# Performance work log

Measured on AMD Instinct MI355X. Metric: run time of the kernel, lower is better.

Reference implementation:

```python
import jax, jax.numpy as jnp
import numpy as np

B, T, D = 1, 2048, 2048
H, HKV, DH = 32, 8, 64          # head_dim = D // H, n_rep = H // HKV
NREP = H // HKV
WINDOW = 1024
NMETA = 128
EPS = 1e-6
ROPE_BASE = 10000.0


def _rmsnorm(x, w):
    # per-head-dim RMSNorm computed in float32 (matches torch module)
    xf = x.astype(jnp.float32)
    rms = jax.lax.rsqrt(jnp.mean(xf * xf, axis=-1, keepdims=True) + EPS)
    return (w * xf * rms).astype(x.dtype)


def _rope(x, pos):
    # x: [B, h, L, DH], pos: [B, L]; interleaved even/odd rotation
    inv_freq = 1.0 / (ROPE_BASE ** (jnp.arange(0, DH, 2, dtype=jnp.float32) / DH))
    freqs = pos.astype(jnp.float32)[..., None] * inv_freq        # [B, L, DH/2]
    cos = jnp.cos(freqs)[:, None]                                # [B, 1, L, DH/2]
    sin = jnp.sin(freqs)[:, None]
    x1, x2 = x[..., ::2], x[..., 1::2]
    rot = jnp.stack([x1 * cos - x2 * sin, x1 * sin + x2 * cos], axis=-1)
    return rot.reshape(x.shape)


def setup_inputs() -> dict:
    key = jax.random.key(0)
    ks = jax.random.split(key, 5)
    s = 0.02
    return {
        "hidden_states": jax.random.normal(ks[0], (B, T, D), jnp.float32),
        "position_ids": jnp.arange(T, dtype=jnp.int32),
        "Wq": jax.random.normal(ks[1], (H * DH, D), jnp.float32) * s,
        "Wk": jax.random.normal(ks[2], (HKV * DH, D), jnp.float32) * s,
        "Wv": jax.random.normal(ks[3], (HKV * DH, D), jnp.float32) * s,
        "Wo": jax.random.normal(ks[4], (D, H * DH), jnp.float32) * s,
        "q_norm_w": jnp.ones((DH,), jnp.float32),
        "k_norm_w": jnp.ones((DH,), jnp.float32),
    }


def reference(hidden_states, position_ids, Wq, Wk, Wv, Wo, q_norm_w, k_norm_w):
    Bn, Tn, _ = hidden_states.shape
    # projections (nn.Linear: x @ W.T)
    q = (hidden_states @ Wq.T).reshape(Bn, Tn, H, DH).transpose(0, 2, 1, 3)   # [B,H,T,DH]
    k = (hidden_states @ Wk.T).reshape(Bn, Tn, HKV, DH).transpose(0, 2, 1, 3)  # [B,HKV,T,DH]
    v = (hidden_states @ Wv.T).reshape(Bn, Tn, HKV, DH).transpose(0, 2, 1, 3)
    q = _rmsnorm(q, q_norm_w)
    k = _rmsnorm(k, k_norm_w)

    Tk = k.shape[2]  # no kv_cache -> Tk == T
    pos_q = position_ids if position_ids.ndim == 2 else jnp.broadcast_to(position_ids[None], (Bn, Tn))
    pos_k = jnp.broadcast_to(jnp.arange(Tk, dtype=jnp.int32)[None], (Bn, Tk))
    q = _rope(q, pos_q[:, -Tn:])
    k = _rope(k, pos_k)

    # GQA repeat_kv
    k = jnp.broadcast_to(k[:, :, None], (Bn, HKV, NREP, Tk, DH)).reshape(Bn, H, Tk, DH)
    v = jnp.broadcast_to(v[:, :, None], (Bn, HKV, NREP, Tk, DH)).reshape(Bn, H, Tk, DH)

    scores = jnp.einsum('bhqd,bhkd->bhqk', q, k) * (DH ** -0.5)

    # sliding-window + meta-token mask (matches _make_swa_mask)
    q_idx = jnp.arange(Tn)[:, None]
    k_idx = jnp.arange(Tk)[None, :]
    offset = Tk - Tn
    abs_q = q_idx + offset
    win_start = jnp.maximum(abs_q - WINDOW + 1, NMETA)
    allowed = ((k_idx >= win_start) & (k_idx <= abs_q)) | (k_idx < NMETA)
    scores = jnp.where(allowed[None, None], scores, -jnp.inf)

    probs = jax.nn.softmax(scores, axis=-1)
    out = jnp.einsum('bhqk,bhkd->bhqd', probs, v)
    out = out.transpose(0, 2, 1, 3).reshape(Bn, Tn, H * DH)
    return out @ Wo.T
```

## Files before the change

### kernel.cpp

```cpp
#include <hip/hip_runtime.h>
#include <hip/hip_bf16.h>
#include <cstdint>

#define TSEQ 2048
#define DMODEL 2048
#define NHEAD 32
#define NKV 8
#define DHEAD 64
#define QKVN 3072
#define AON 2048

using bf16x8 = __attribute__((ext_vector_type(8))) short;
using bf16x4 = __attribute__((ext_vector_type(4))) short;
using f32x4  = __attribute__((ext_vector_type(4))) float;

__device__ __forceinline__ ushort f2bf(float f) {
  union { float f; uint32_t u; } v; v.f = f;
  uint32_t u = v.u;
  return (ushort)((u + 0x7fffu + ((u >> 16) & 1u)) >> 16);
}

__device__ __forceinline__ float bf2f(ushort u) {
  union { uint32_t u; float f; } v; v.u = ((uint32_t)u) << 16;
  return v.f;
}

__device__ __forceinline__ float fexp2(float x) {
#if __has_builtin(__builtin_amdgcn_exp2f)
  return __builtin_amdgcn_exp2f(x);
#else
  return __expf(x * 0.69314718055994531f);
#endif
}

__device__ __forceinline__ uint32_t cvtpk(float lo, float hi) {
  uint32_t r;
  asm("v_cvt_pk_bf16_f32 %0, %1, %2" : "=v"(r) : "v"(lo), "v"(hi));
  return r;
}

__device__ __forceinline__ void gload16(const void* g, void* l) {
  __builtin_amdgcn_global_load_lds((const __attribute__((address_space(1))) void*)g,
                                   (__attribute__((address_space(3))) void*)l,
                                   16, 0, 0);
}

#define RG0 1048576
#define RG1 2097152
#define RG2 2359296
#define RG3 2621440
#define RG4 3670016
__global__ void k_cvt_all(const float* __restrict__ X, const float* __restrict__ Wq,
                          const float* __restrict__ Wk, const float* __restrict__ Wv,
                          const float* __restrict__ Wo,
                          ushort* __restrict__ Xb, ushort* __restrict__ Wqkvb,
                          ushort* __restrict__ Wob) {
  int idx = blockIdx.x * blockDim.x + threadIdx.x;
  int stride = gridDim.x * blockDim.x;
  for (int i = idx; i < RG4; i += stride) {
    const float4* s; ushort4* d;
    if (i < RG0)      { s = (const float4*)X  + i;         d = (ushort4*)Xb + i; }
    else if (i < RG1) { s = (const float4*)Wq + (i - RG0); d = (ushort4*)Wqkvb + (i - RG0); }
    else if (i < RG2) { s = (const float4*)Wk + (i - RG1); d = (ushort4*)Wqkvb + 1048576 + (i - RG1); }
    else if (i < RG3) { s = (const float4*)Wv + (i - RG2); d = (ushort4*)Wqkvb + 1310720 + (i - RG2); }
    else              { s = (const float4*)Wo + (i - RG3); d = (ushort4*)Wob + (i - RG3); }
    float4 v = *s;
    ushort4 o;
    o.x = f2bf(v.x); o.y = f2bf(v.y); o.z = f2bf(v.z); o.w = f2bf(v.w);
    *d = o;
  }
}

template <bool BF16OUT>
__global__ __launch_bounds__(256) void k_gemm128(
    const ushort* __restrict__ A, const ushort* __restrict__ B,
    void* __restrict__ Cv, int M, int N, int K)
{
  __shared__ ushort As[4][128 * 32];
  __shared__ ushort Bs[4][128 * 32];
  const int m0 = blockIdx.y * 128, n0 = blockIdx.x * 128;
  const int tid = threadIdx.x;
  const int w = tid >> 6, lane = tid & 63, lg = lane >> 4, lr = lane & 15;
  const int wr = (w >> 1) * 64, wc = (w & 1) * 64;

  f32x4 acc[4][4];
#pragma unroll
  for (int i = 0; i < 4; ++i)
#pragma unroll
    for (int j = 0; j < 4; ++j) acc[i][j] = (f32x4){0.f, 0.f, 0.f, 0.f};

  const int nt = K >> 5;

  auto stage = [&](int b, int t) {
    const int k0 = t << 5;
#pragma unroll
    for (int j = 0; j < 2; ++j) {
      int ci = j * 256 + tid;
      int row = ci >> 2, c = ci & 3;
      int clog = c ^ ((row >> 1) & 3);
      gload16(A + (size_t)(m0 + row) * K + k0 + clog * 8, As[b] + ci * 8);
      gload16(B + (size_t)(n0 + row) * K + k0 + clog * 8, Bs[b] + ci * 8);
    }
  };

  stage(0, 0); stage(1, 1); stage(2, 2);

  for (int t = 0; t < nt; ++t) {
    int rem = nt - t;
    if (rem >= 3)      asm volatile("s_waitcnt vmcnt(8)" ::: "memory");
    else if (rem == 2) asm volatile("s_waitcnt vmcnt(4)" ::: "memory");
    else               asm volatile("s_waitcnt vmcnt(0)" ::: "memory");
    __builtin_amdgcn_s_barrier();
    __builtin_amdgcn_sched_barrier(0);

    const ushort* as = As[t & 3];
    const ushort* bs = Bs[t & 3];
    bf16x8 af[4], bfr[4];
#pragma unroll
    for (int i = 0; i < 4; ++i) {
      int ra = wr + i * 16 + lr;
      int rb = wc + i * 16 + lr;
      af[i]  = *reinterpret_cast<const bf16x8*>(as + ra * 32 + ((lg ^ ((ra >> 1) & 3)) << 3));
      bfr[i] = *reinterpret_cast<const bf16x8*>(bs + rb * 32 + ((lg ^ ((rb >> 1) & 3)) << 3));
    }
    asm volatile("s_waitcnt lgkmcnt(0)" ::: "memory");
    __builtin_amdgcn_sched_barrier(0);

    if (t + 3 < nt) stage((t + 3) & 3, t + 3);

#pragma unroll
    for (int i = 0; i < 4; ++i)
#pragma unroll
      for (int j = 0; j < 4; ++j)
        acc[i][j] = __builtin_amdgcn_mfma_f32_16x16x32_bf16(af[i], bfr[j], acc[i][j], 0, 0, 0);
  }

#pragma unroll
  for (int i = 0; i < 4; ++i)
#pragma unroll
    for (int j = 0; j < 4; ++j)
#pragma unroll
      for (int r = 0; r < 4; ++r) {
        size_t idx = (size_t)(m0 + wr + i * 16 + lg * 4 + r) * N + n0 + wc + j * 16 + lr;
        if (BF16OUT) ((ushort*)Cv)[idx] = f2bf(acc[i][j][r]);
        else         ((float*)Cv)[idx] = acc[i][j][r];
      }
}

template <bool BF16OUT>
__global__ __launch_bounds__(256) void k_gemm64(
    const ushort* __restrict__ A, const ushort* __restrict__ B,
    void* __restrict__ Cv, int M, int N, int K)
{
  __shared__ ushort As[4][64 * 32];
  __shared__ ushort Bs[4][128 * 32];
  const int m0 = blockIdx.y * 64, n0 = blockIdx.x * 128;
  const int tid = threadIdx.x;
  const int w = tid >> 6, lane = tid & 63, lg = lane >> 4, lr = lane & 15;
  const int wr = (w >> 1) * 32, wc = (w & 1) * 64;

  f32x4 acc[2][4];
#pragma unroll
  for (int i = 0; i < 2; ++i)
#pragma unroll
    for (int j = 0; j < 4; ++j) acc[i][j] = (f32x4){0.f, 0.f, 0.f, 0.f};

  const int nt = K >> 5;

  auto stage = [&](int b, int t) {
    const int k0 = t << 5;
    {
      int ci = tid;
      int row = ci >> 2, c = ci & 3;
      int clog = c ^ ((row >> 1) & 3);
      gload16(A + (size_t)(m0 + row) * K + k0 + clog * 8, As[b] + ci * 8);
    }
#pragma unroll
    for (int j = 0; j < 2; ++j) {
      int ci = j * 256 + tid;
      int row = ci >> 2, c = ci & 3;
      int clog = c ^ ((row >> 1) & 3);
      gload16(B + (size_t)(n0 + row) * K + k0 + clog * 8, Bs[b] + ci * 8);
    }
  };

  stage(0, 0); stage(1, 1); stage(2, 2);

  for (int t = 0; t < nt; ++t) {
    int rem = nt - t;
    if (rem >= 3)      asm volatile("s_waitcnt vmcnt(6)" ::: "memory");
    else if (rem == 2) asm volatile("s_waitcnt vmcnt(3)" ::: "memory");
    else               asm volatile("s_waitcnt vmcnt(0)" ::: "memory");
    __builtin_amdgcn_s_barrier();
    __builtin_amdgcn_sched_barrier(0);

    const ushort* as = As[t & 3];
    const ushort* bs = Bs[t & 3];
    bf16x8 af[2], bfr[4];
#pragma unroll
    for (int i = 0; i < 2; ++i) {
      int ra = wr + i * 16 + lr;
      af[i] = *reinterpret_cast<const bf16x8*>(as + ra * 32 + ((lg ^ ((ra >> 1) & 3)) << 3));
    }
#pragma unroll
    for (int j = 0; j < 4; ++j) {
      int rb = wc + j * 16 + lr;
      bfr[j] = *reinterpret_cast<const bf16x8*>(bs + rb * 32 + ((lg ^ ((rb >> 1) & 3)) << 3));
    }
    asm volatile("s_waitcnt lgkmcnt(0)" ::: "memory");
    __builtin_amdgcn_sched_barrier(0);

    if (t + 3 < nt) stage((t + 3) & 3, t + 3);

#pragma unroll
    for (int i = 0; i < 2; ++i)
#pragma unroll
      for (int j = 0; j < 4; ++j)
        acc[i][j] = __builtin_amdgcn_mfma_f32_16x16x32_bf16(af[i], bfr[j], acc[i][j], 0, 0, 0);
  }

#pragma unroll
  for (int i = 0; i < 2; ++i)
#pragma unroll
    for (int j = 0; j < 4; ++j)
#pragma unroll
      for (int r = 0; r < 4; ++r) {
        size_t idx = (size_t)(m0 + wr + i * 16 + lg * 4 + r) * N + n0 + wc + j * 16 + lr;
        if (BF16OUT) ((ushort*)Cv)[idx] = f2bf(acc[i][j][r]);
        else         ((float*)Cv)[idx] = acc[i][j][r];
      }
}

__global__ __launch_bounds__(256) void k_normrope(
    const ushort* __restrict__ qkv, const int* __restrict__ pos,
    const float* __restrict__ qw, const float* __restrict__ kw,
    ushort* __restrict__ Qb, ushort* __restrict__ Kb, ushort* __restrict__ Vt)
{
  int gw = blockIdx.x * 4 + (threadIdx.x >> 6);
  int lane = threadIdx.x & 63;
  int t = gw / 48, u = gw % 48;
  if (t >= TSEQ) return;
  if (u < 40) {
    int col = (u < 32) ? u * 64 + lane : 2048 + (u - 32) * 64 + lane;
    float x = bf2f(qkv[(size_t)t * QKVN + col]);
    float ss = x * x;
#pragma unroll
    for (int mm = 32; mm; mm >>= 1) ss += __shfl_xor(ss, mm);
    float r = rsqrtf(ss * (1.0f / 64.0f) + 1e-6f);
    x = x * r * ((u < 32) ? qw[lane] : kw[lane]);
    int p = (u < 32) ? pos[t] : t;
    int j = lane >> 1;
    float invf = fexp2((float)j * (-0.41524101186092029f));
    float s, c;
    __sincosf((float)p * invf, &s, &c);
    float other = __shfl_xor(x, 1);
    float out = (lane & 1) ? (other * s + x * c) : (x * c - other * s);
    if (u < 32)
      Qb[((size_t)u * TSEQ + t) * 64 + lane] = f2bf(out * 0.18033688011112043f);
    else
      Kb[((size_t)(u - 32) * TSEQ + t) * 64 + lane] = f2bf(out);
  } else {
    int hv = u - 40;
    Vt[((size_t)hv * 64 + lane) * TSEQ + t] = qkv[(size_t)t * QKVN + 2560 + hv * 64 + lane];
  }
}

__global__ __launch_bounds__(512) void k_attn(
    const ushort* __restrict__ Qb, const ushort* __restrict__ Kb,
    const ushort* __restrict__ Vt, ushort* __restrict__ AO)
{
  __shared__ ushort Ks[2][64 * 64];
  __shared__ ushort Vs[2][64 * 64];

  const int h = blockIdx.x;
  const int q0 = ((int)gridDim.y - 1 - (int)blockIdx.y) * 128;
  const int tid = threadIdx.x;
  const int w = tid >> 6, lane = tid & 63;
  const int lg = lane >> 4, lr = lane & 15;
  const int qrow = q0 + w * 16 + lr;

  const ushort* qp = Qb + ((size_t)h * TSEQ + qrow) * 64;
  const bf16x8 qf0 = *reinterpret_cast<const bf16x8*>(qp + lg * 8);
  const bf16x8 qf1 = *reinterpret_cast<const bf16x8*>(qp + 32 + lg * 8);
  const int hk = h >> 2;
  const char* Kh = (const char*)(Kb + (size_t)hk * TSEQ * 64);
  const char* Vh = (const char*)(Vt + (size_t)hk * 64 * TSEQ);

  float m = -1e30f, lsum = 0.0f;
  f32x4 o[4];
#pragma unroll
  for (int dt = 0; dt < 4; ++dt) o[dt] = (f32x4){0.f, 0.f, 0.f, 0.f};

  const int wlo = (q0 >= 1152) ? (q0 - 1024) : 128;
  int nwin = (q0 + 64 - wlo) / 64 + 1;
  if (nwin < 0) nwin = 0;
  const int ntiles = 2 + nwin;
  const int qw0 = q0 + w * 16;
  const int wmaxstart = ((qw0 + 15 - 1023) > 128) ? (qw0 + 15 - 1023) : 128;
  const int wminstart = ((qw0 - 1023) > 128) ? (qw0 - 1023) : 128;
  const int wstart_lane = ((qrow - 1023) > 128) ? (qrow - 1023) : 128;

  auto stage = [&](int b, int kb) {
    int off = tid * 16;
    int r = off >> 7, bp = off & 127;
    int bs = bp ^ ((r & 7) << 4);
    gload16(Kh + (size_t)(kb + r) * 128 + bs, (char*)Ks[b] + off);
    gload16(Vh + (size_t)r * (TSEQ * 2) + (size_t)kb * 2 + bs, (char*)Vs[b] + off);
  };

  stage(0, 0);

  for (int ti = 0; ti < ntiles; ++ti) {
    const int kb = (ti < 2) ? ti * 64 : wlo + (ti - 2) * 64;
    __syncthreads();
    if (ti + 1 < ntiles) {
      const int kb1 = (ti + 1 < 2) ? (ti + 1) * 64 : wlo + (ti - 1) * 64;
      stage((ti + 1) & 1, kb1);
    }
    if (ti >= 2 && ((kb > qw0 + 15) || (kb + 63 < wminstart))) continue;

    const char* ks = (const char*)Ks[ti & 1];
    const char* vs = (const char*)Vs[ti & 1];
    const bool needmask = (ti >= 2) && !((kb + 63 <= qw0) && (kb >= wmaxstart));

    f32x4 st[4];
#pragma unroll
    for (int s = 0; s < 4; ++s) {
      int row = s * 16 + lr;
      int sw = (row & 7) << 4;
      bf16x8 kf0 = *reinterpret_cast<const bf16x8*>(ks + row * 128 + ((lg * 16) ^ sw));
      bf16x8 kf1 = *reinterpret_cast<const bf16x8*>(ks + row * 128 + ((64 + lg * 16) ^ sw));
      f32x4 acc = (f32x4){0.f, 0.f, 0.f, 0.f};
      acc = __builtin_amdgcn_mfma_f32_16x16x32_bf16(kf0, qf0, acc, 0, 0, 0);
      acc = __builtin_amdgcn_mfma_f32_16x16x32_bf16(kf1, qf1, acc, 0, 0, 0);
      st[s] = acc;
    }
    if (needmask) {
#pragma unroll
      for (int s = 0; s < 4; ++s)
#pragma unroll
        for (int r = 0; r < 4; ++r) {
          int key = kb + s * 16 + lg * 4 + r;
          bool ok = (key >= wstart_lane) && (key <= qrow);
          if (!ok) st[s][r] = -1e30f;
        }
    }
    float pmax = st[0][0];
#pragma unroll
    for (int s = 0; s < 4; ++s)
#pragma unroll
      for (int r = 0; r < 4; ++r) pmax = fmaxf(pmax, st[s][r]);
    pmax = fmaxf(pmax, __shfl_xor(pmax, 16));
    pmax = fmaxf(pmax, __shfl_xor(pmax, 32));

    const bool defer = __all(pmax <= m + 8.0f);
    if (!defer) {
      float mnew = fmaxf(m, pmax);
      float sc = fexp2(m - mnew);
      m = mnew;
      lsum *= sc;
#pragma unroll
      for (int dt = 0; dt < 4; ++dt) o[dt] = o[dt] * sc;
    }

    float psum = 0.f;
    bf16x4 pb[4];
#pragma unroll
    for (int s = 0; s < 4; ++s) {
      float e0 = fexp2(st[s][0] - m);
      float e1 = fexp2(st[s][1] - m);
      float e2 = fexp2(st[s][2] - m);
      float e3 = fexp2(st[s][3] - m);
      psum += (e0 + e1) + (e2 + e3);
      union { uint32_t u[2]; bf16x4 b; } pk;
      pk.u[0] = cvtpk(e0, e1);
      pk.u[1] = cvtpk(e2, e3);
      pb[s] = pk.b;
    }
    psum += __shfl_xor(psum, 16);
    psum += __shfl_xor(psum, 32);
    lsum += psum;

#pragma unroll
    for (int dt = 0; dt < 4; ++dt) {
      int row = dt * 16 + lr;
      int sw = (row & 7) << 4;
#pragma unroll
      for (int s = 0; s < 4; ++s) {
        bf16x4 vf = *reinterpret_cast<const bf16x4*>(vs + row * 128 + ((s * 32 + lg * 8) ^ sw));
        o[dt] = __builtin_amdgcn_mfma_f32_16x16x16bf16_1k(vf, pb[s], o[dt], 0, 0, 0);
      }
    }
  }

  float inv = 1.0f / lsum;
#pragma unroll
  for (int dt = 0; dt < 4; ++dt)
#pragma unroll
    for (int r = 0; r < 4; ++r)
      AO[(size_t)qrow * AON + h * 64 + dt * 16 + lg * 4 + r] = f2bf(o[dt][r] * inv);
}

extern "C" void kernel_launch(void* const* d_in, const int* in_sizes, int n_in,
                              void* d_out, int out_size, void* d_ws, size_t ws_size,
                              hipStream_t stream) {
  const float* hs = (const float*)d_in[0];
  const int* pos  = (const int*)d_in[1];
  const float* Wq = (const float*)d_in[2];
  const float* Wk = (const float*)d_in[3];
  const float* Wv = (const float*)d_in[4];
  const float* Wo = (const float*)d_in[5];
  const float* qw = (const float*)d_in[6];
  const float* kw = (const float*)d_in[7];
  float* out = (float*)d_out;

  char* ws = (char*)d_ws;
  ushort* Xb    = (ushort*)ws; ws += (size_t)2048 * 2048 * 2;
  ushort* Wqkvb = (ushort*)ws; ws += (size_t)3072 * 2048 * 2;
  ushort* Wob   = (ushort*)ws; ws += (size_t)2048 * 2048 * 2;
  ushort* QKVb  = (ushort*)ws; ws += (size_t)2048 * 3072 * 2;
  ushort* Qb    = (ushort*)ws; ws += (size_t)32 * 2048 * 64 * 2;
  ushort* Kb    = (ushort*)ws; ws += (size_t)8 * 2048 * 64 * 2;
  ushort* Vt    = (ushort*)ws; ws += (size_t)8 * 64 * 2048 * 2;
  ushort* AO    = (ushort*)ws;

  k_cvt_all<<<2048, 256, 0, stream>>>(hs, Wq, Wk, Wv, Wo, Xb, Wqkvb, Wob);

  k_gemm128<true><<<dim3(QKVN / 128, TSEQ / 128), 256, 0, stream>>>(Xb, Wqkvb, QKVb, TSEQ, QKVN, DMODEL);
  k_normrope<<<(TSEQ * 48) / 4, 256, 0, stream>>>(QKVb, pos, qw, kw, Qb, Kb, Vt);
  k_attn<<<dim3(NHEAD, TSEQ / 128), 512, 0, stream>>>(Qb, Kb, Vt, AO);
  k_gemm64<false><<<dim3(DMODEL / 128, TSEQ / 64), 256, 0, stream>>>(AO, Wob, out, TSEQ, DMODEL, AON);
}
```

Measured before the change: 137.5 us.

## Fuse RMSNorm, RoPE and V transpose into QKV GEMM epilogue

Removes the separate norm/rope kernel and the intermediate bf16 QKV buffer. The QKV GEMM epilogue now does per-head RMSNorm with shuffle reductions, applies RoPE and writes Q/K/Vt directly. A sin/cos table is precomputed inside the conversion kernel. This saves one launch and a write plus read of the QKV activations. In exchange the GEMM epilogue gets heavier, the Vt stores are strided and uncoalesced, and every element reads the table.

```diff
diff --git a/kernel.cpp b/kernel.cpp
--- a/kernel.cpp
+++ b/kernel.cpp
@@ -20,11 +20,6 @@
   return (ushort)((u + 0x7fffu + ((u >> 16) & 1u)) >> 16);
 }
 
-__device__ __forceinline__ float bf2f(ushort u) {
-  union { uint32_t u; float f; } v; v.u = ((uint32_t)u) << 16;
-  return v.f;
-}
-
 __device__ __forceinline__ float fexp2(float x) {
 #if __has_builtin(__builtin_amdgcn_exp2f)
   return __builtin_amdgcn_exp2f(x);
@@ -52,12 +47,20 @@
 #define RG4 3670016
 __global__ void k_cvt_all(const float* __restrict__ X, const float* __restrict__ Wq,
                           const float* __restrict__ Wk, const float* __restrict__ Wv,
-                          const float* __restrict__ Wo,
+                          const float* __restrict__ Wo, const int* __restrict__ pos,
                           ushort* __restrict__ Xb, ushort* __restrict__ Wqkvb,
-                          ushort* __restrict__ Wob) {
-  int idx = blockIdx.x * blockDim.x + threadIdx.x;
+                          ushort* __restrict__ Wob, float4* __restrict__ Tbl) {
+  int gid = blockIdx.x * blockDim.x + threadIdx.x;
+  if (gid < TSEQ * 32) {
+    int t = gid >> 5, jj = gid & 31;
+    float invf = fexp2((float)jj * (-0.41524101186092029f));
+    float qs, qc, ks, kc;
+    __sincosf((float)pos[t] * invf, &qs, &qc);
+    __sincosf((float)t * invf, &ks, &kc);
+    Tbl[gid] = make_float4(qc * 0.18033688011112043f, qs * 0.18033688011112043f, kc, ks);
+  }
   int stride = gridDim.x * blockDim.x;
-  for (int i = idx; i < RG4; i += stride) {
+  for (int i = gid; i < RG4; i += stride) {
     const float4* s; ushort4* d;
     if (i < RG0)      { s = (const float4*)X  + i;         d = (ushort4*)Xb + i; }
     else if (i < RG1) { s = (const float4*)Wq + (i - RG0); d = (ushort4*)Wqkvb + (i - RG0); }
@@ -71,10 +74,12 @@
   }
 }
 
-template <bool BF16OUT>
-__global__ __launch_bounds__(256) void k_gemm128(
+__global__ __launch_bounds__(256) void k_gemm_qkv(
     const ushort* __restrict__ A, const ushort* __restrict__ B,
-    void* __restrict__ Cv, int M, int N, int K)
+    const float* __restrict__ qw, const float* __restrict__ kw,
+    const float4* __restrict__ Tbl,
+    ushort* __restrict__ Qb, ushort* __restrict__ Kb, ushort* __restrict__ Vt,
+    int M, int N, int K)
 {
   __shared__ ushort As[4][128 * 32];
   __shared__ ushort Bs[4][128 * 32];
@@ -135,22 +140,54 @@
         acc[i][j] = __builtin_amdgcn_mfma_f32_16x16x32_bf16(af[i], bfr[j], acc[i][j], 0, 0, 0);
   }
 
-#pragma unroll
-  for (int i = 0; i < 4; ++i)
-#pragma unroll
-    for (int j = 0; j < 4; ++j)
+  const int colunit = (n0 + wc) >> 6;
+  if (colunit < 40) {
+    const bool isQ = (colunit < 32);
+    const float* wn = isQ ? qw : kw;
+    float wv[4];
+#pragma unroll
+    for (int j = 0; j < 4; ++j) wv[j] = wn[j * 16 + lr];
+    ushort* dst = isQ ? (Qb + (size_t)colunit * TSEQ * 64)
+                      : (Kb + (size_t)(colunit - 32) * TSEQ * 64);
+#pragma unroll
+    for (int i = 0; i < 4; ++i)
 #pragma unroll
       for (int r = 0; r < 4; ++r) {
-        size_t idx = (size_t)(m0 + wr + i * 16 + lg * 4 + r) * N + n0 + wc + j * 16 + lr;
-        if (BF16OUT) ((ushort*)Cv)[idx] = f2bf(acc[i][j][r]);
-        else         ((float*)Cv)[idx] = acc[i][j][r];
+        int row = m0 + wr + i * 16 + lg * 4 + r;
+        float ss = 0.f;
+#pragma unroll
+        for (int j = 0; j < 4; ++j) { float x = acc[i][j][r]; ss += x * x; }
+        ss += __shfl_xor(ss, 1); ss += __shfl_xor(ss, 2);
+        ss += __shfl_xor(ss, 4); ss += __shfl_xor(ss, 8);
+        float rms = rsqrtf(ss * (1.0f / 64.0f) + 1e-6f);
+#pragma unroll
+        for (int j = 0; j < 4; ++j) {
+          float xh = acc[i][j][r] * rms * wv[j];
+          float other = __shfl_xor(xh, 1);
+          float4 tb = Tbl[(size_t)row * 32 + j * 8 + (lr >> 1)];
+          float c = isQ ? tb.x : tb.z;
+          float s = isQ ? tb.y : tb.w;
+          float outv = (lr & 1) ? (other * s + xh * c) : (xh * c - other * s);
+          dst[(size_t)row * 64 + j * 16 + lr] = f2bf(outv);
+        }
       }
-}
-
-template <bool BF16OUT>
+  } else {
+    const int hv = colunit - 40;
+#pragma unroll
+    for (int i = 0; i < 4; ++i)
+#pragma unroll
+      for (int j = 0; j < 4; ++j)
+#pragma unroll
+        for (int r = 0; r < 4; ++r) {
+          int row = m0 + wr + i * 16 + lg * 4 + r;
+          Vt[((size_t)hv * 64 + j * 16 + lr) * TSEQ + row] = f2bf(acc[i][j][r]);
+        }
+  }
+}
+
 __global__ __launch_bounds__(256) void k_gemm64(
     const ushort* __restrict__ A, const ushort* __restrict__ B,
-    void* __restrict__ Cv, int M, int N, int K)
+    float* __restrict__ C, int M, int N, int K)
 {
   __shared__ ushort As[4][64 * 32];
   __shared__ ushort Bs[4][128 * 32];
@@ -224,45 +261,8 @@
 #pragma unroll
     for (int j = 0; j < 4; ++j)
 #pragma unroll
-      for (int r = 0; r < 4; ++r) {
-        size_t idx = (size_t)(m0 + wr + i * 16 + lg * 4 + r) * N + n0 + wc + j * 16 + lr;
-        if (BF16OUT) ((ushort*)Cv)[idx] = f2bf(acc[i][j][r]);
-        else         ((float*)Cv)[idx] = acc[i][j][r];
-      }
-}
-
-__global__ __launch_bounds__(256) void k_normrope(
-    const ushort* __restrict__ qkv, const int* __restrict__ pos,
-    const float* __restrict__ qw, const float* __restrict__ kw,
-    ushort* __restrict__ Qb, ushort* __restrict__ Kb, ushort* __restrict__ Vt)
-{
-  int gw = blockIdx.x * 4 + (threadIdx.x >> 6);
-  int lane = threadIdx.x & 63;
-  int t = gw / 48, u = gw % 48;
-  if (t >= TSEQ) return;
-  if (u < 40) {
-    int col = (u < 32) ? u * 64 + lane : 2048 + (u - 32) * 64 + lane;
-    float x = bf2f(qkv[(size_t)t * QKVN + col]);
-    float ss = x * x;
-#pragma unroll
-    for (int mm = 32; mm; mm >>= 1) ss += __shfl_xor(ss, mm);
-    float r = rsqrtf(ss * (1.0f / 64.0f) + 1e-6f);
-    x = x * r * ((u < 32) ? qw[lane] : kw[lane]);
-    int p = (u < 32) ? pos[t] : t;
-    int j = lane >> 1;
-    float invf = fexp2((float)j * (-0.41524101186092029f));
-    float s, c;
-    __sincosf((float)p * invf, &s, &c);
-    float other = __shfl_xor(x, 1);
-    float out = (lane & 1) ? (other * s + x * c) : (x * c - other * s);
-    if (u < 32)
-      Qb[((size_t)u * TSEQ + t) * 64 + lane] = f2bf(out * 0.18033688011112043f);
-    else
-      Kb[((size_t)(u - 32) * TSEQ + t) * 64 + lane] = f2bf(out);
-  } else {
-    int hv = u - 40;
-    Vt[((size_t)hv * 64 + lane) * TSEQ + t] = qkv[(size_t)t * QKVN + 2560 + hv * 64 + lane];
-  }
+      for (int r = 0; r < 4; ++r)
+        C[(size_t)(m0 + wr + i * 16 + lg * 4 + r) * N + n0 + wc + j * 16 + lr] = acc[i][j][r];
 }
 
 __global__ __launch_bounds__(512) void k_attn(
@@ -418,16 +418,16 @@
   ushort* Xb    = (ushort*)ws; ws += (size_t)2048 * 2048 * 2;
   ushort* Wqkvb = (ushort*)ws; ws += (size_t)3072 * 2048 * 2;
   ushort* Wob   = (ushort*)ws; ws += (size_t)2048 * 2048 * 2;
-  ushort* QKVb  = (ushort*)ws; ws += (size_t)2048 * 3072 * 2;
+  float4* Tbl   = (float4*)ws; ws += (size_t)2048 * 32 * 16;
   ushort* Qb    = (ushort*)ws; ws += (size_t)32 * 2048 * 64 * 2;
   ushort* Kb    = (ushort*)ws; ws += (size_t)8 * 2048 * 64 * 2;
   ushort* Vt    = (ushort*)ws; ws += (size_t)8 * 64 * 2048 * 2;
   ushort* AO    = (ushort*)ws;
 
-  k_cvt_all<<<2048, 256, 0, stream>>>(hs, Wq, Wk, Wv, Wo, Xb, Wqkvb, Wob);
-
-  k_gemm128<true><<<dim3(QKVN / 128, TSEQ / 128), 256, 0, stream>>>(Xb, Wqkvb, QKVb, TSEQ, QKVN, DMODEL);
-  k_normrope<<<(TSEQ * 48) / 4, 256, 0, stream>>>(QKVb, pos, qw, kw, Qb, Kb, Vt);
+  k_cvt_all<<<2048, 256, 0, stream>>>(hs, Wq, Wk, Wv, Wo, pos, Xb, Wqkvb, Wob, Tbl);
+
+  k_gemm_qkv<<<dim3(QKVN / 128, TSEQ / 128), 256, 0, stream>>>(
+      Xb, Wqkvb, qw, kw, Tbl, Qb, Kb, Vt, TSEQ, QKVN, DMODEL);
   k_attn<<<dim3(NHEAD, TSEQ / 128), 512, 0, stream>>>(Qb, Kb, Vt, AO);
-  k_gemm64<false><<<dim3(DMODEL / 128, TSEQ / 64), 256, 0, stream>>>(AO, Wob, out, TSEQ, DMODEL, AON);
-}
+  k_gemm64<<<dim3(DMODEL / 128, TSEQ / 64), 256, 0, stream>>>(AO, Wob, out, TSEQ, DMODEL, AON);
+}
```

Result: faster. 125.0 us (-9.1%).
